# Performance work log

Hardware: AMD Instinct MI355X
Metric: run time of the kernel (lower is better)

## Reference

```python
import jax, jax.numpy as jnp
import numpy as np

KH, KW = 3, 3
SH, SW = 1, 1
DH, DW = 1, 1
OFFSET_GROUPS = 1
WEIGHT_GROUPS = 1


def setup_inputs() -> dict:
    key = jax.random.key(0)
    k1, k2, k3, k4 = jax.random.split(key, 4)
    B, C, H, W = 8, 128, 64, 64
    F = 128
    x = jax.random.normal(k1, (B, C, H, W), dtype=jnp.float32)
    offset = jax.random.normal(k2, (B, OFFSET_GROUPS * 2 * KH * KW, H, W), dtype=jnp.float32)
    mask = jax.random.uniform(k3, (B, OFFSET_GROUPS * KH * KW, H, W), dtype=jnp.float32)
    weight = jax.random.normal(k4, (F, C // WEIGHT_GROUPS, KH, KW), dtype=jnp.float32) * 0.05
    return {"x": x, "offset": offset, "mask": mask, "weight": weight}


def _deform_conv2d(x, offset, mask, weight):
    B, C, H, W = x.shape
    F = weight.shape[0]
    Ho, Wo = offset.shape[2], offset.shape[3]
    KK = KH * KW
    og = OFFSET_GROUPS
    Cg = C // og

    # SAME padding (TF convention, symmetric-ish: extra pad at bottom/right)
    pad_h = max((Ho - 1) * SH + (KH - 1) * DH + 1 - H, 0)
    pad_w = max((Wo - 1) * SW + (KW - 1) * DW + 1 - W, 0)
    pad_t, pad_l = pad_h // 2, pad_w // 2

    # offsets laid out as [B, og, KK, (dy,dx), Ho, Wo]
    off = offset.reshape(B, og, KK, 2, Ho, Wo)
    dy, dx = off[:, :, :, 0], off[:, :, :, 1]  # [B, og, KK, Ho, Wo]

    ki, kj = jnp.meshgrid(jnp.arange(KH), jnp.arange(KW), indexing="ij")
    ki = ki.reshape(KK)
    kj = kj.reshape(KK)
    base_y = (jnp.arange(Ho) * SH - pad_t)[None, :] + (ki * DH)[:, None]  # [KK, Ho]
    base_x = (jnp.arange(Wo) * SW - pad_l)[None, :] + (kj * DW)[:, None]  # [KK, Wo]

    py = base_y[None, None, :, :, None].astype(x.dtype) + dy  # [B, og, KK, Ho, Wo]
    px = base_x[None, None, :, None, :].astype(x.dtype) + dx

    y0 = jnp.floor(py)
    x0 = jnp.floor(px)
    ly = py - y0  # fractional parts
    lx = px - x0
    hy = 1.0 - ly
    hx = 1.0 - lx
    y0i = y0.astype(jnp.int32)
    x0i = x0.astype(jnp.int32)

    xg = x.reshape(B, og, Cg, H * W)

    def gather_corner(yi, xi):
        valid = (yi >= 0) & (yi < H) & (xi >= 0) & (xi < W)  # [B, og, KK, Ho, Wo]
        yc = jnp.clip(yi, 0, H - 1)
        xc = jnp.clip(xi, 0, W - 1)
        flat = (yc * W + xc).reshape(B, og, 1, KK * Ho * Wo)
        vals = jnp.take_along_axis(xg, flat, axis=3).reshape(B, og, Cg, KK, Ho, Wo)
        return vals * valid[:, :, None].astype(x.dtype)

    v00 = gather_corner(y0i, x0i)
    v01 = gather_corner(y0i, x0i + 1)
    v10 = gather_corner(y0i + 1, x0i)
    v11 = gather_corner(y0i + 1, x0i + 1)

    w00 = (hy * hx)[:, :, None]
    w01 = (hy * lx)[:, :, None]
    w10 = (ly * hx)[:, :, None]
    w11 = (ly * lx)[:, :, None]
    sampled = v00 * w00 + v01 * w01 + v10 * w10 + v11 * w11  # [B, og, Cg, KK, Ho, Wo]

    # modulation mask: [B, og, KK, Ho, Wo]
    m = mask.reshape(B, og, KK, Ho, Wo)
    sampled = sampled * m[:, :, None]

    # grouped matmul (weight_groups=1 -> plain); columns ordered c*KK + kk, matching
    # weight [F, C, KH, KW] flattened.
    cols = sampled.reshape(B, C * KK, Ho, Wo)
    out = jnp.einsum("fk,bkhw->bfhw", weight.reshape(F, C // WEIGHT_GROUPS * KK), cols)
    return out


def reference(x, offset, mask, weight):
    return _deform_conv2d(x, offset, mask, weight)
```

## Files before the change

### kernel.cpp

```cpp
#include <hip/hip_runtime.h>
#include <hip/hip_bf16.h>

typedef __attribute__((ext_vector_type(8))) short bf16x8;
typedef __attribute__((ext_vector_type(4))) float f32x4;
typedef __attribute__((ext_vector_type(2))) float f32x2;
typedef unsigned int uint32;
typedef unsigned short ushort_t;
typedef __attribute__((ext_vector_type(4))) uint32 u32x4;

#define SB0() __builtin_amdgcn_sched_barrier(0)
#define VMCNT(N) do { asm volatile("s_waitcnt vmcnt(" #N ")" ::: "memory"); SB0(); } while (0)

__device__ __forceinline__ ushort_t f2bf(float f) {
    unsigned int u = __float_as_uint(f);
    u = (u + 0x7FFFu + ((u >> 16) & 1u)) >> 16;
    return (ushort_t)u;
}

__device__ __forceinline__ uint32 cvt_pk_bf16(float lo, float hi) {
    uint32 r;
    asm("v_cvt_pk_bf16_f32 %0, %1, %2" : "=v"(r) : "v"(lo), "v"(hi));
    return r;
}

template<int IMM>
__device__ __forceinline__ u32x4 gload(const char* p) {
    u32x4 r;
    asm volatile("global_load_dwordx4 %0, %1, off offset:%2"
                 : "=v"(r) : "v"(p), "n"(IMM));
    return r;
}

__device__ __forceinline__ void gload_lds16(const void* g, void* l) {
    __builtin_amdgcn_global_load_lds(
        (const __attribute__((address_space(1))) uint32*)g,
        (__attribute__((address_space(3))) uint32*)l, 16, 0, 0);
}

__global__ __launch_bounds__(256) void prep_all(const float* __restrict__ x,
                                                const float* __restrict__ w,
                                                ushort_t* __restrict__ xt,
                                                ushort_t* __restrict__ wT2) {
    int bi = blockIdx.x;
    int t = threadIdx.x;
    if (bi >= 4096) {
        int idx = (bi - 4096) * 256 + t;
        int j  = idx & 7;
        int p  = (idx >> 3) & 15;
        int lu = (idx >> 7) & 3;
        int ft = (idx >> 9) & 7;
        int ks = (idx >> 12) & 3;
        int tap = idx >> 14;
        int f = ft * 16 + p;
        int c = ks * 32 + lu * 8 + j;
        wT2[idx] = f2bf(w[((size_t)f * 128 + c) * 9 + tap]);
        return;
    }
    __shared__ float tile[32][33];
    int b = bi & 7;
    int r2 = bi >> 3;
    int wb = r2 & 1, cb = (r2 >> 1) & 3, y = r2 >> 3;
    int lw = t & 31, lc = t >> 5;
    #pragma unroll
    for (int pass = 0; pass < 4; ++pass) {
        int c = cb * 32 + lc + pass * 8;
        tile[lc + pass * 8][lw] = x[(((size_t)b * 128 + c) * 64 + y) * 64 + wb * 32 + lw];
    }
    __syncthreads();
    int cc = t & 31, xl = t >> 5;
    #pragma unroll
    for (int pass = 0; pass < 4; ++pass) {
        int xll = xl + pass * 8;
        xt[(((size_t)b * 64 + y) * 64 + wb * 32 + xll) * 128 + cb * 32 + cc] =
            f2bf(tile[cc][xll]);
    }
}

__device__ __forceinline__ bf16x8 interp4(u32x4 c0, u32x4 c1, u32x4 c2, u32x4 c3,
                                          f32x4 wv) {
    uint32 rr[4];
    #pragma unroll
    for (int i = 0; i < 4; ++i) {
        f32x2 a, s;
        uint32 u = c0[i];
        a.x = __uint_as_float(u << 16); a.y = __uint_as_float(u & 0xffff0000u);
        s = a * wv.x;
        u = c1[i];
        a.x = __uint_as_float(u << 16); a.y = __uint_as_float(u & 0xffff0000u);
        s += a * wv.y;
        u = c2[i];
        a.x = __uint_as_float(u << 16); a.y = __uint_as_float(u & 0xffff0000u);
        s += a * wv.z;
        u = c3[i];
        a.x = __uint_as_float(u << 16); a.y = __uint_as_float(u & 0xffff0000u);
        s += a * wv.w;
        rr[i] = cvt_pk_bf16(s.x, s.y);
    }
    u32x4 q = {rr[0], rr[1], rr[2], rr[3]};
    return __builtin_bit_cast(bf16x8, q);
}

__global__ __launch_bounds__(256, 2) void dcn_main(
    const float* __restrict__ offset, const float* __restrict__ mask,
    const ushort_t* __restrict__ xt, const ushort_t* __restrict__ wT2,
    float* __restrict__ out)
{
    __shared__ ushort_t Abuf[2][16384];
    __shared__ float  pws_l[9][64][4];
    __shared__ uint32 pos_l[9][64];

    int bi = blockIdx.x;
    int b = bi & 7, ho = bi >> 3;
    int t = threadIdx.x, lane = t & 63, wid = t >> 6;
    int p = lane & 15, lu = lane >> 4;
    int pix = wid * 16 + p;

    {
        const ushort_t* s0 = wT2 + t * 8;
        #pragma unroll
        for (int r = 0; r < 8; ++r)
            gload_lds16(s0 + r * 2048, &Abuf[0][(r * 256 + t) * 8]);
    }
    for (int item = t; item < 576; item += 256) {
        int k = item >> 6, pi = item & 63;
        int ki = k / 3, kj = k - ki * 3;
        float dy = offset[(((size_t)b * 18 + 2 * k)     * 64 + ho) * 64 + pi];
        float dx = offset[(((size_t)b * 18 + 2 * k + 1) * 64 + ho) * 64 + pi];
        float m  = mask  [(((size_t)b * 9  + k)         * 64 + ho) * 64 + pi];
        float py = (float)(ho - 1 + ki) + dy;
        float px = (float)(pi - 1 + kj) + dx;
        float y0f = floorf(py), x0f = floorf(px);
        float ly = py - y0f, lx = px - x0f;
        float hy = 1.f - ly, hx = 1.f - lx;
        int y0 = (int)y0f, x0 = (int)x0f;
        int y1 = y0 + 1, x1 = x0 + 1;
        float vy0 = (y0 >= 0 && y0 < 64) ? 1.f : 0.f;
        float vy1 = (y1 >= 0 && y1 < 64) ? 1.f : 0.f;
        float vx0 = (x0 >= 0 && x0 < 64) ? 1.f : 0.f;
        float vx1 = (x1 >= 0 && x1 < 64) ? 1.f : 0.f;
        pws_l[k][pi][0] = hy * hx * m * vy0 * vx0;
        pws_l[k][pi][1] = hy * lx * m * vy0 * vx1;
        pws_l[k][pi][2] = ly * hx * m * vy1 * vx0;
        pws_l[k][pi][3] = ly * lx * m * vy1 * vx1;
        int y0c = min(max(y0, 0), 63), y1c = min(max(y1, 0), 63);
        int x0c = min(max(x0, 0), 63), x1c = min(max(x1, 0), 63);
        pos_l[k][pi] = (uint32)(y0c * 64 + x0c) | ((uint32)(y1c * 64 + x1c) << 16);
    }
    asm volatile("s_waitcnt vmcnt(0)" ::: "memory");
    __syncthreads();

    const char* xb = (const char*)xt + (size_t)b * (64 * 64 * 256);
    f32x4 acc[8];
    #pragma unroll
    for (int i = 0; i < 8; ++i) acc[i] = (f32x4){0.f, 0.f, 0.f, 0.f};

    const char *p00, *p01, *p10, *p11;
    f32x4 wv;
    auto tap_params = [&](int k, const char*& q00, const char*& q01,
                          const char*& q10, const char*& q11, f32x4& w4) {
        uint32 pp = pos_l[k][pix];
        w4 = *(const f32x4*)pws_l[k][pix];
        int i00 = pp & 0xffffu, i11 = pp >> 16;
        int o00 = i00 << 8, o11 = i11 << 8;
        int o01 = ((i00 & 0xffc0u) | (i11 & 63u)) << 8;
        int o10 = ((i11 & 0xffc0u) | (i00 & 63u)) << 8;
        int cl = lu * 16;
        q00 = xb + o00 + cl; q01 = xb + o01 + cl;
        q10 = xb + o10 + cl; q11 = xb + o11 + cl;
    };

    tap_params(0, p00, p01, p10, p11, wv);
    u32x4 g0 = gload<0>(p00), g1 = gload<0>(p01), g2 = gload<0>(p10), g3 = gload<0>(p11);
    SB0();

    #define MFMA_KS(KS, BF, AB)                                                  \
        do {                                                                     \
            _Pragma("unroll")                                                    \
            for (int ft = 0; ft < 8; ++ft) {                                     \
                bf16x8 aa = *(const bf16x8*)&(AB)[(((KS) * 8 + ft) * 64 + lane) * 8]; \
                acc[ft] = __builtin_amdgcn_mfma_f32_16x16x32_bf16(aa, (BF), acc[ft], 0, 0, 0); \
            }                                                                    \
        } while (0)

    #pragma unroll 1
    for (int tap = 0; tap < 8; ++tap) {
        const ushort_t* Ab = &Abuf[tap & 1][0];
        ushort_t* An = &Abuf[(tap + 1) & 1][0];
        u32x4 h0 = gload<64>(p00), h1 = gload<64>(p01), h2 = gload<64>(p10), h3 = gload<64>(p11);
        {
            const ushort_t* ss = wT2 + (size_t)(tap + 1) * 16384 + t * 8;
            #pragma unroll
            for (int r = 0; r < 8; ++r)
                gload_lds16(ss + r * 2048, &An[(r * 256 + t) * 8]);
        }
        SB0();
        VMCNT(12);
        {
            bf16x8 bf = interp4(g0, g1, g2, g3, wv);
            MFMA_KS(0, bf, Ab);
        }
        u32x4 i0 = gload<128>(p00), i1 = gload<128>(p01), i2 = gload<128>(p10), i3 = gload<128>(p11);
        SB0();
        VMCNT(12);
        {
            bf16x8 bf = interp4(h0, h1, h2, h3, wv);
            MFMA_KS(1, bf, Ab);
        }
        u32x4 j0 = gload<192>(p00), j1 = gload<192>(p01), j2 = gload<192>(p10), j3 = gload<192>(p11);
        SB0();
        VMCNT(4);
        {
            bf16x8 bf = interp4(i0, i1, i2, i3, wv);
            MFMA_KS(2, bf, Ab);
        }
        const char *q00, *q01, *q10, *q11;
        f32x4 wv2;
        tap_params(tap + 1, q00, q01, q10, q11, wv2);
        g0 = gload<0>(q00); g1 = gload<0>(q01); g2 = gload<0>(q10); g3 = gload<0>(q11);
        SB0();
        VMCNT(4);
        {
            bf16x8 bf = interp4(j0, j1, j2, j3, wv);
            MFMA_KS(3, bf, Ab);
        }
        p00 = q00; p01 = q01; p10 = q10; p11 = q11; wv = wv2;
        SB0();
        __builtin_amdgcn_s_barrier();
        SB0();
    }

    {
        const ushort_t* Ab = &Abuf[0][0];
        u32x4 h0 = gload<64>(p00), h1 = gload<64>(p01), h2 = gload<64>(p10), h3 = gload<64>(p11);
        SB0();
        VMCNT(4);
        { bf16x8 bf = interp4(g0, g1, g2, g3, wv); MFMA_KS(0, bf, Ab); }
        u32x4 i0 = gload<128>(p00), i1 = gload<128>(p01), i2 = gload<128>(p10), i3 = gload<128>(p11);
        SB0();
        VMCNT(4);
        { bf16x8 bf = interp4(h0, h1, h2, h3, wv); MFMA_KS(1, bf, Ab); }
        u32x4 j0 = gload<192>(p00), j1 = gload<192>(p01), j2 = gload<192>(p10), j3 = gload<192>(p11);
        SB0();
        VMCNT(4);
        { bf16x8 bf = interp4(i0, i1, i2, i3, wv); MFMA_KS(2, bf, Ab); }
        VMCNT(0);
        { bf16x8 bf = interp4(j0, j1, j2, j3, wv); MFMA_KS(3, bf, Ab); }
    }

    float* outb = out + (size_t)b * 128 * 4096 + ho * 64 + wid * 16 + p;
    #pragma unroll
    for (int ft = 0; ft < 8; ++ft)
        #pragma unroll
        for (int r = 0; r < 4; ++r) {
            int f = ft * 16 + lu * 4 + r;
            outb[(size_t)f * 4096] = acc[ft][r];
        }
    #undef MFMA_KS
}

extern "C" void kernel_launch(void* const* d_in, const int* in_sizes, int n_in,
                              void* d_out, int out_size, void* d_ws, size_t ws_size,
                              hipStream_t stream) {
    const float* x      = (const float*)d_in[0];
    const float* offset = (const float*)d_in[1];
    const float* mask   = (const float*)d_in[2];
    const float* weight = (const float*)d_in[3];
    float* out = (float*)d_out;

    ushort_t* xt  = (ushort_t*)d_ws;
    ushort_t* wT2 = xt + (size_t)8 * 64 * 64 * 128;
    if (ws_size < (size_t)(8 * 64 * 64 * 128 + 9 * 16384) * 2) return;

    prep_all<<<4672, 256, 0, stream>>>(x, weight, xt, wT2);
    dcn_main<<<512, 256, 0, stream>>>(offset, mask, xt, wT2, out);
}
```

Measured before the change: 50.50 us.

## Split channel reduction across two wave groups with 512-thread blocks and LDS reduce

Doubles the block to 512 threads so two wave groups each take half of the channel k-steps per tap for the same 16-pixel strips. Each group gathers its half of the four bilinear corners up front, and the partial accumulators are summed through LDS at the end. The old staggered per-k-step load pipeline with partial vmcnt waits becomes a simpler issue-all then wait-all scheme, with the next tap prefetched during the MFMAs. This adds an LDS reduction and a full vmcnt(0) wait per tap. The tighter launch bound of 512 threads and 4 blocks may force register spills.

```diff
diff --git a/kernel.cpp b/kernel.cpp
--- a/kernel.cpp
+++ b/kernel.cpp
@@ -9,7 +9,7 @@
 typedef __attribute__((ext_vector_type(4))) uint32 u32x4;
 
 #define SB0() __builtin_amdgcn_sched_barrier(0)
-#define VMCNT(N) do { asm volatile("s_waitcnt vmcnt(" #N ")" ::: "memory"); SB0(); } while (0)
+#define VMCNT0() do { asm volatile("s_waitcnt vmcnt(0)" ::: "memory"); SB0(); } while (0)
 
 __device__ __forceinline__ ushort_t f2bf(float f) {
     unsigned int u = __float_as_uint(f);
@@ -100,7 +100,7 @@
     return __builtin_bit_cast(bf16x8, q);
 }
 
-__global__ __launch_bounds__(256, 2) void dcn_main(
+__global__ __launch_bounds__(512, 4) void dcn_main(
     const float* __restrict__ offset, const float* __restrict__ mask,
     const ushort_t* __restrict__ xt, const ushort_t* __restrict__ wT2,
     float* __restrict__ out)
@@ -112,16 +112,17 @@
     int bi = blockIdx.x;
     int b = bi & 7, ho = bi >> 3;
     int t = threadIdx.x, lane = t & 63, wid = t >> 6;
+    int strip = wid & 3, tg = wid >> 2;
     int p = lane & 15, lu = lane >> 4;
-    int pix = wid * 16 + p;
+    int pix = strip * 16 + p;
 
     {
         const ushort_t* s0 = wT2 + t * 8;
         #pragma unroll
-        for (int r = 0; r < 8; ++r)
-            gload_lds16(s0 + r * 2048, &Abuf[0][(r * 256 + t) * 8]);
-    }
-    for (int item = t; item < 576; item += 256) {
+        for (int r = 0; r < 4; ++r)
+            gload_lds16(s0 + r * 4096, &Abuf[0][(r * 512 + t) * 8]);
+    }
+    for (int item = t; item < 576; item += 512) {
         int k = item >> 6, pi = item & 63;
         int ki = k / 3, kj = k - ki * 3;
         float dy = offset[(((size_t)b * 18 + 2 * k)     * 64 + ho) * 64 + pi];
@@ -146,116 +147,103 @@
         int x0c = min(max(x0, 0), 63), x1c = min(max(x1, 0), 63);
         pos_l[k][pi] = (uint32)(y0c * 64 + x0c) | ((uint32)(y1c * 64 + x1c) << 16);
     }
-    asm volatile("s_waitcnt vmcnt(0)" ::: "memory");
     __syncthreads();
 
     const char* xb = (const char*)xt + (size_t)b * (64 * 64 * 256);
+    uint32 cl = (uint32)(tg * 128 + lu * 16);
+
     f32x4 acc[8];
     #pragma unroll
     for (int i = 0; i < 8; ++i) acc[i] = (f32x4){0.f, 0.f, 0.f, 0.f};
 
+    f32x4 wv;
     const char *p00, *p01, *p10, *p11;
-    f32x4 wv;
-    auto tap_params = [&](int k, const char*& q00, const char*& q01,
-                          const char*& q10, const char*& q11, f32x4& w4) {
+    auto tap_params = [&](int k) {
         uint32 pp = pos_l[k][pix];
-        w4 = *(const f32x4*)pws_l[k][pix];
-        int i00 = pp & 0xffffu, i11 = pp >> 16;
-        int o00 = i00 << 8, o11 = i11 << 8;
-        int o01 = ((i00 & 0xffc0u) | (i11 & 63u)) << 8;
-        int o10 = ((i11 & 0xffc0u) | (i00 & 63u)) << 8;
-        int cl = lu * 16;
-        q00 = xb + o00 + cl; q01 = xb + o01 + cl;
-        q10 = xb + o10 + cl; q11 = xb + o11 + cl;
+        wv = *(const f32x4*)pws_l[k][pix];
+        uint32 i00 = pp & 0xffffu, i11 = pp >> 16;
+        uint32 o01 = (i00 & 0xffc0u) | (i11 & 63u);
+        uint32 o10 = (i11 & 0xffc0u) | (i00 & 63u);
+        p00 = xb + ((i00 << 8) + cl); p01 = xb + ((o01 << 8) + cl);
+        p10 = xb + ((o10 << 8) + cl); p11 = xb + ((i11 << 8) + cl);
     };
 
-    tap_params(0, p00, p01, p10, p11, wv);
-    u32x4 g0 = gload<0>(p00), g1 = gload<0>(p01), g2 = gload<0>(p10), g3 = gload<0>(p11);
+    u32x4 g[4][2];
+    #define ISSUE_G()                          \
+        do {                                   \
+            g[0][0] = gload<0>(p00);           \
+            g[0][1] = gload<64>(p00);          \
+            g[1][0] = gload<0>(p01);           \
+            g[1][1] = gload<64>(p01);          \
+            g[2][0] = gload<0>(p10);           \
+            g[2][1] = gload<64>(p10);          \
+            g[3][0] = gload<0>(p11);           \
+            g[3][1] = gload<64>(p11);          \
+        } while (0)
+
+    tap_params(0);
+    ISSUE_G();
     SB0();
-
-    #define MFMA_KS(KS, BF, AB)                                                  \
-        do {                                                                     \
-            _Pragma("unroll")                                                    \
-            for (int ft = 0; ft < 8; ++ft) {                                     \
-                bf16x8 aa = *(const bf16x8*)&(AB)[(((KS) * 8 + ft) * 64 + lane) * 8]; \
-                acc[ft] = __builtin_amdgcn_mfma_f32_16x16x32_bf16(aa, (BF), acc[ft], 0, 0, 0); \
-            }                                                                    \
-        } while (0)
+    VMCNT0();
 
     #pragma unroll 1
-    for (int tap = 0; tap < 8; ++tap) {
+    for (int tap = 0; tap < 9; ++tap) {
+        bf16x8 b0 = interp4(g[0][0], g[1][0], g[2][0], g[3][0], wv);
+        bf16x8 b1 = interp4(g[0][1], g[1][1], g[2][1], g[3][1], wv);
+
+        if (tap < 8) {
+            ushort_t* An = &Abuf[(tap + 1) & 1][0];
+            const ushort_t* ss = wT2 + (size_t)(tap + 1) * 16384 + t * 8;
+            #pragma unroll
+            for (int r = 0; r < 4; ++r)
+                gload_lds16(ss + r * 4096, &An[(r * 512 + t) * 8]);
+            tap_params(tap + 1);
+            ISSUE_G();
+            SB0();
+        }
+
         const ushort_t* Ab = &Abuf[tap & 1][0];
-        ushort_t* An = &Abuf[(tap + 1) & 1][0];
-        u32x4 h0 = gload<64>(p00), h1 = gload<64>(p01), h2 = gload<64>(p10), h3 = gload<64>(p11);
-        {
-            const ushort_t* ss = wT2 + (size_t)(tap + 1) * 16384 + t * 8;
-            #pragma unroll
-            for (int r = 0; r < 8; ++r)
-                gload_lds16(ss + r * 2048, &An[(r * 256 + t) * 8]);
+        #pragma unroll
+        for (int q = 0; q < 2; ++q) {
+            int ks = tg * 2 + q;
+            bf16x8 bb = q ? b1 : b0;
+            #pragma unroll
+            for (int ft = 0; ft < 8; ++ft) {
+                bf16x8 aa = *(const bf16x8*)&Ab[((ks * 8 + ft) * 64 + lane) * 8];
+                acc[ft] = __builtin_amdgcn_mfma_f32_16x16x32_bf16(aa, bb, acc[ft], 0, 0, 0);
+            }
         }
-        SB0();
-        VMCNT(12);
-        {
-            bf16x8 bf = interp4(g0, g1, g2, g3, wv);
-            MFMA_KS(0, bf, Ab);
+
+        if (tap < 8) {
+            VMCNT0();
+            __builtin_amdgcn_s_barrier();
+            SB0();
         }
-        u32x4 i0 = gload<128>(p00), i1 = gload<128>(p01), i2 = gload<128>(p10), i3 = gload<128>(p11);
-        SB0();
-        VMCNT(12);
-        {
-            bf16x8 bf = interp4(h0, h1, h2, h3, wv);
-            MFMA_KS(1, bf, Ab);
-        }
-        u32x4 j0 = gload<192>(p00), j1 = gload<192>(p01), j2 = gload<192>(p10), j3 = gload<192>(p11);
-        SB0();
-        VMCNT(4);
-        {
-            bf16x8 bf = interp4(i0, i1, i2, i3, wv);
-            MFMA_KS(2, bf, Ab);
-        }
-        const char *q00, *q01, *q10, *q11;
-        f32x4 wv2;
-        tap_params(tap + 1, q00, q01, q10, q11, wv2);
-        g0 = gload<0>(q00); g1 = gload<0>(q01); g2 = gload<0>(q10); g3 = gload<0>(q11);
-        SB0();
-        VMCNT(4);
-        {
-            bf16x8 bf = interp4(j0, j1, j2, j3, wv);
-            MFMA_KS(3, bf, Ab);
-        }
-        p00 = q00; p01 = q01; p10 = q10; p11 = q11; wv = wv2;
-        SB0();
-        __builtin_amdgcn_s_barrier();
-        SB0();
-    }
-
-    {
-        const ushort_t* Ab = &Abuf[0][0];
-        u32x4 h0 = gload<64>(p00), h1 = gload<64>(p01), h2 = gload<64>(p10), h3 = gload<64>(p11);
-        SB0();
-        VMCNT(4);
-        { bf16x8 bf = interp4(g0, g1, g2, g3, wv); MFMA_KS(0, bf, Ab); }
-        u32x4 i0 = gload<128>(p00), i1 = gload<128>(p01), i2 = gload<128>(p10), i3 = gload<128>(p11);
-        SB0();
-        VMCNT(4);
-        { bf16x8 bf = interp4(h0, h1, h2, h3, wv); MFMA_KS(1, bf, Ab); }
-        u32x4 j0 = gload<192>(p00), j1 = gload<192>(p01), j2 = gload<192>(p10), j3 = gload<192>(p11);
-        SB0();
-        VMCNT(4);
-        { bf16x8 bf = interp4(i0, i1, i2, i3, wv); MFMA_KS(2, bf, Ab); }
-        VMCNT(0);
-        { bf16x8 bf = interp4(j0, j1, j2, j3, wv); MFMA_KS(3, bf, Ab); }
-    }
-
-    float* outb = out + (size_t)b * 128 * 4096 + ho * 64 + wid * 16 + p;
-    #pragma unroll
-    for (int ft = 0; ft < 8; ++ft)
-        #pragma unroll
-        for (int r = 0; r < 4; ++r) {
-            int f = ft * 16 + lu * 4 + r;
-            outb[(size_t)f * 4096] = acc[ft][r];
-        }
-    #undef MFMA_KS
+    }
+    #undef ISSUE_G
+
+    __syncthreads();
+    float* red = (float*)&Abuf[0][0];
+    if (tg == 1) {
+        #pragma unroll
+        for (int ft = 0; ft < 8; ++ft)
+            #pragma unroll
+            for (int r = 0; r < 4; ++r) {
+                int f = ft * 16 + lu * 4 + r;
+                red[(strip * 128 + f) * 17 + p] = acc[ft][r];
+            }
+    }
+    __syncthreads();
+    if (tg == 0) {
+        float* outb = out + (size_t)b * 128 * 4096 + ho * 64 + strip * 16 + p;
+        #pragma unroll
+        for (int ft = 0; ft < 8; ++ft)
+            #pragma unroll
+            for (int r = 0; r < 4; ++r) {
+                int f = ft * 16 + lu * 4 + r;
+                outb[(size_t)f * 4096] = acc[ft][r] + red[(strip * 128 + f) * 17 + p];
+            }
+    }
 }
 
 extern "C" void kernel_launch(void* const* d_in, const int* in_sizes, int n_in,
@@ -272,5 +260,5 @@
     if (ws_size < (size_t)(8 * 64 * 64 * 128 + 9 * 16384) * 2) return;
 
     prep_all<<<4672, 256, 0, stream>>>(x, weight, xt, wT2);
-    dcn_main<<<512, 256, 0, stream>>>(offset, mask, xt, wT2, out);
-}
+    dcn_main<<<512, 512, 0, stream>>>(offset, mask, xt, wT2, out);
+}
```

Result: slower. 53.89 us (+6.7%).
